# Performance work log

Hardware: AMD Instinct MI355X
Metric: run time of the kernel (lower is better)

The kernel has to match this reference:

```python
import jax, jax.numpy as jnp
import numpy as np

B, L, D, DA, NL = 32, 2048, 512, 512, 512

def setup_inputs() -> dict:
    key = jax.random.key(0)
    k1, k2, k3, k4 = jax.random.split(key, 4)
    std = 0.03
    return {
        "x": jax.random.normal(k1, (B, L, D), dtype=jnp.float32),
        "W1": jax.random.normal(k2, (DA, D), dtype=jnp.float32) * std,   # first_linears[0].weight [d_a, size]
        "W2": jax.random.normal(k3, (NL, DA), dtype=jnp.float32) * std,  # second_linears[0].weight [n_labels, d_a]
        "W3": jax.random.normal(k4, (NL, D), dtype=jnp.float32) * std,   # third_linears[0].weight [n_labels, size]
        "b3": jnp.zeros((NL,), dtype=jnp.float32),                        # third_linears[0].bias
    }

def reference(x, W1, W2, W3, b3):
    # weights = tanh(first_linear(x)) : [B, L, DA]
    w = jnp.tanh(jnp.einsum("bld,ad->bla", x, W1))
    # att logits : [B, L, NL]; softmax over seq dim (dim=1), then transpose -> [B, NL, L]
    att = jax.nn.softmax(jnp.einsum("bla,na->bln", w, W2), axis=1)
    att_weights = jnp.swapaxes(att, 1, 2)  # [B, NL, L]
    # context_vector = att_weights @ x : [B, NL, D]
    context_vector = jnp.einsum("bnl,bld->bnd", att_weights, x)
    # label-wise diagonal mul-sum-add: [B, NL]
    weighted_output = jnp.einsum("bnd,nd->bn", context_vector, W3) + b3
    return (context_vector, weighted_output, att_weights)
```

## Files before the change

kernel.cpp:

```cpp
#include <hip/hip_runtime.h>
#include <math.h>

#define BB 32
#define LL 2048
#define DD 512
#define DA_ 512
#define NL_ 512

typedef __bf16 bf16;
typedef __bf16 bf16x8 __attribute__((ext_vector_type(8)));
typedef __bf16 bf16x4 __attribute__((ext_vector_type(4)));
typedef float floatx4 __attribute__((ext_vector_type(4)));

__device__ __forceinline__ void dma16(const void* g, void* l) {
    __builtin_amdgcn_global_load_lds((__attribute__((address_space(1))) void*)g,
                                     (__attribute__((address_space(3))) void*)l,
                                     16, 0, 0);
}

__device__ __forceinline__ float fast_tanh(float x) {
    const float e = __expf(2.f * x);
    return 1.f - 2.f * __builtin_amdgcn_rcpf(e + 1.f);
}

__device__ __forceinline__ void gemm_core(const bf16* __restrict__ A,
                                          const bf16* __restrict__ B,
                                          int K, int lda, int ldb,
                                          floatx4 acc[4][4])
{
    __shared__ bf16 As[2][128 * 32];
    __shared__ bf16 Bs[2][128 * 32];
    const int tid = threadIdx.x;
    const int lane = tid & 63, wv = tid >> 6;
    const int wr = wv >> 1, wc = wv & 1;
    const int lm = lane & 15, quad = lane >> 4;

    const bf16* a0 = A + (size_t)(tid >> 2) * lda + (tid & 3) * 8;
    const bf16* b0 = B + (size_t)(tid >> 2) * ldb + (tid & 3) * 8;
    const size_t a1 = (size_t)64 * lda, b1 = (size_t)64 * ldb;

    dma16(a0,      &As[0][tid * 8]);
    dma16(a0 + a1, &As[0][2048 + tid * 8]);
    dma16(b0,      &Bs[0][tid * 8]);
    dma16(b0 + b1, &Bs[0][2048 + tid * 8]);
    __syncthreads();

    const int nk = K >> 5;
    for (int t = 0; t < nk; ++t) {
        const int cur = t & 1;
        if (t + 1 < nk) {
            const int k0 = (t + 1) << 5;
            dma16(a0 + k0,      &As[cur ^ 1][tid * 8]);
            dma16(a0 + a1 + k0, &As[cur ^ 1][2048 + tid * 8]);
            dma16(b0 + k0,      &Bs[cur ^ 1][tid * 8]);
            dma16(b0 + b1 + k0, &Bs[cur ^ 1][2048 + tid * 8]);
        }
        bf16x8 af[4], bfr[4];
        #pragma unroll
        for (int tt = 0; tt < 4; ++tt) {
            af[tt]  = *(const bf16x8*)(&As[cur][(wr * 64 + tt * 16 + lm) * 32 + quad * 8]);
            bfr[tt] = *(const bf16x8*)(&Bs[cur][(wc * 64 + tt * 16 + lm) * 32 + quad * 8]);
        }
        __builtin_amdgcn_s_setprio(1);
        #pragma unroll
        for (int i = 0; i < 4; ++i)
            #pragma unroll
            for (int j = 0; j < 4; ++j)
                acc[i][j] = __builtin_amdgcn_mfma_f32_16x16x32_bf16(af[i], bfr[j], acc[i][j], 0, 0, 0);
        __builtin_amdgcn_s_setprio(0);
        __syncthreads();
    }
}

__global__ __launch_bounds__(256) void k_cvt(const float* __restrict__ src,
                                             bf16* __restrict__ dst, int n)
{
    const int i = (blockIdx.x * 256 + threadIdx.x) * 4;
    if (i < n) {
        const float4 v = *(const float4*)(src + i);
        bf16x4 p = {(bf16)v.x, (bf16)v.y, (bf16)v.z, (bf16)v.w};
        *(bf16x4*)(dst + i) = p;
    }
}

__global__ __launch_bounds__(256) void k_init_wo(const float* __restrict__ b3,
                                                 float* __restrict__ wo)
{
    const int i = blockIdx.x * 256 + threadIdx.x;
    wo[i] = b3[i & (NL_ - 1)];
}

__global__ __launch_bounds__(256) void k_transpose(const float* __restrict__ x,
                                                   bf16* __restrict__ xT,
                                                   bf16* __restrict__ xb)
{
    __shared__ float T[64][68];
    const int b = blockIdx.z;
    const int l0 = blockIdx.x * 64, d0 = blockIdx.y * 64;
    const int tid = threadIdx.x;
    const float* xsrc = x + ((size_t)b * LL + l0) * DD + d0;
    bf16* xbdst = xb + ((size_t)b * LL + l0) * DD + d0;
    #pragma unroll
    for (int it = 0; it < 4; ++it) {
        const int c = tid + it * 256;
        const int lr = c >> 4, cc = (c & 15) * 4;
        const float4 v = *(const float4*)(xsrc + (size_t)lr * DD + cc);
        T[lr][cc] = v.x; T[lr][cc + 1] = v.y; T[lr][cc + 2] = v.z; T[lr][cc + 3] = v.w;
        bf16x4 p = {(bf16)v.x, (bf16)v.y, (bf16)v.z, (bf16)v.w};
        *(bf16x4*)(xbdst + (size_t)lr * DD + cc) = p;
    }
    __syncthreads();
    const int dl = tid >> 2, ls = (tid & 3) * 16;
    bf16x8 p0, p1;
    #pragma unroll
    for (int j = 0; j < 8; ++j) p0[j] = (bf16)T[ls + j][dl];
    #pragma unroll
    for (int j = 0; j < 8; ++j) p1[j] = (bf16)T[ls + 8 + j][dl];
    bf16* o = xT + ((size_t)b * DD + d0 + dl) * LL + l0 + ls;
    *(bf16x8*)o = p0;
    *(bf16x8*)(o + 8) = p1;
}

__global__ __launch_bounds__(256) void k_gemm1(const bf16* __restrict__ xb,
                                               const bf16* __restrict__ W1b,
                                               bf16* __restrict__ wb)
{
    const int n0 = blockIdx.x * 128;
    const size_t m0 = (size_t)blockIdx.y * 128;
    floatx4 acc[4][4];
    #pragma unroll
    for (int i = 0; i < 4; ++i)
        #pragma unroll
        for (int j = 0; j < 4; ++j) { floatx4 z = {0.f, 0.f, 0.f, 0.f}; acc[i][j] = z; }
    gemm_core(xb + m0 * DD, W1b + (size_t)n0 * DD, DD, DD, DD, acc);

    const int tid = threadIdx.x, lane = tid & 63, wv = tid >> 6;
    const int wr = wv >> 1, wc = wv & 1, lm = lane & 15, quad = lane >> 4;
    const size_t row0 = m0 + wr * 64 + quad * 4;
    const int col0 = n0 + wc * 64 + lm;
    #pragma unroll
    for (int i = 0; i < 4; ++i)
        #pragma unroll
        for (int j = 0; j < 4; ++j)
            #pragma unroll
            for (int r = 0; r < 4; ++r)
                wb[(row0 + i * 16 + r) * DA_ + col0 + j * 16] = (bf16)fast_tanh(acc[i][j][r]);
}

__global__ __launch_bounds__(256) void k_gemm2(const bf16* __restrict__ wb,
                                               const bf16* __restrict__ W2b,
                                               bf16* __restrict__ logitsb)
{
    const int c0 = blockIdx.x * 128;
    const int m0 = blockIdx.y * 128;
    floatx4 acc[4][4];
    #pragma unroll
    for (int i = 0; i < 4; ++i)
        #pragma unroll
        for (int j = 0; j < 4; ++j) { floatx4 z = {0.f, 0.f, 0.f, 0.f}; acc[i][j] = z; }
    gemm_core(W2b + (size_t)m0 * DA_, wb + (size_t)c0 * DA_, DA_, DA_, DA_, acc);

    const int b = c0 >> 11, lloc = c0 & (LL - 1);
    const int tid = threadIdx.x, lane = tid & 63, wv = tid >> 6;
    const int wr = wv >> 1, wc = wv & 1, lm = lane & 15, quad = lane >> 4;
    bf16* base = logitsb + ((size_t)b * NL_ + m0 + wr * 64 + quad * 4) * LL
               + lloc + wc * 64 + lm;
    #pragma unroll
    for (int i = 0; i < 4; ++i)
        #pragma unroll
        for (int j = 0; j < 4; ++j)
            #pragma unroll
            for (int r = 0; r < 4; ++r)
                base[(size_t)(i * 16 + r) * LL + j * 16] = (bf16)acc[i][j][r];
}

__global__ __launch_bounds__(256) void k_softmax(const bf16* __restrict__ logitsb,
                                                 float* __restrict__ att,
                                                 bf16* __restrict__ attb)
{
    const int tid = threadIdx.x;
    const bf16* p = logitsb + (size_t)blockIdx.x * LL;
    float* po = att + (size_t)blockIdx.x * LL;
    bf16* pb = attb + (size_t)blockIdx.x * LL;

    const bf16x8 v = *(const bf16x8*)(p + tid * 8);
    float f[8];
    #pragma unroll
    for (int j = 0; j < 8; ++j) f[j] = (float)v[j];

    __shared__ float red[8];
    float m = f[0];
    #pragma unroll
    for (int j = 1; j < 8; ++j) m = fmaxf(m, f[j]);
    #pragma unroll
    for (int off = 32; off; off >>= 1) m = fmaxf(m, __shfl_down(m, off));
    if ((tid & 63) == 0) red[tid >> 6] = m;
    __syncthreads();
    m = fmaxf(fmaxf(red[0], red[1]), fmaxf(red[2], red[3]));

    float s = 0.f;
    #pragma unroll
    for (int j = 0; j < 8; ++j) { f[j] = __expf(f[j] - m); s += f[j]; }
    #pragma unroll
    for (int off = 32; off; off >>= 1) s += __shfl_down(s, off);
    if ((tid & 63) == 0) red[4 + (tid >> 6)] = s;
    __syncthreads();
    s = red[4] + red[5] + red[6] + red[7];

    const float inv = 1.0f / s;
    float4 o0, o1;
    o0.x = f[0] * inv; o0.y = f[1] * inv; o0.z = f[2] * inv; o0.w = f[3] * inv;
    o1.x = f[4] * inv; o1.y = f[5] * inv; o1.z = f[6] * inv; o1.w = f[7] * inv;
    *(float4*)(po + tid * 8) = o0;
    *(float4*)(po + tid * 8 + 4) = o1;
    bf16x8 q = {(bf16)o0.x, (bf16)o0.y, (bf16)o0.z, (bf16)o0.w,
                (bf16)o1.x, (bf16)o1.y, (bf16)o1.z, (bf16)o1.w};
    *(bf16x8*)(pb + tid * 8) = q;
}

__global__ __launch_bounds__(256) void k_gemm3(const bf16* __restrict__ attb,
                                               const bf16* __restrict__ xT,
                                               float* __restrict__ ctx,
                                               const float* __restrict__ W3,
                                               float* __restrict__ wo)
{
    const int b = blockIdx.z;
    const int n0 = blockIdx.x * 128;
    const int m0 = blockIdx.y * 128;
    floatx4 acc[4][4];
    #pragma unroll
    for (int i = 0; i < 4; ++i)
        #pragma unroll
        for (int j = 0; j < 4; ++j) { floatx4 z = {0.f, 0.f, 0.f, 0.f}; acc[i][j] = z; }
    gemm_core(attb + ((size_t)b * NL_ + m0) * LL,
              xT + ((size_t)b * DD + n0) * LL, LL, LL, LL, acc);

    const int tid = threadIdx.x, lane = tid & 63, wv = tid >> 6;
    const int wr = wv >> 1, wc = wv & 1, lm = lane & 15, quad = lane >> 4;
    float* base = ctx + ((size_t)b * NL_ + m0 + wr * 64 + quad * 4) * DD
                + n0 + wc * 64 + lm;
    #pragma unroll
    for (int i = 0; i < 4; ++i)
        #pragma unroll
        for (int j = 0; j < 4; ++j)
            #pragma unroll
            for (int r = 0; r < 4; ++r)
                base[(size_t)(i * 16 + r) * DD + j * 16] = acc[i][j][r];

    const int nbase = m0 + wr * 64 + quad * 4;
    const int dbase = n0 + wc * 64 + lm;
    #pragma unroll
    for (int i = 0; i < 4; ++i) {
        #pragma unroll
        for (int r = 0; r < 4; ++r) {
            const int n = nbase + i * 16 + r;
            float s = 0.f;
            #pragma unroll
            for (int j = 0; j < 4; ++j)
                s += acc[i][j][r] * W3[(size_t)n * DD + dbase + j * 16];
            #pragma unroll
            for (int off = 8; off; off >>= 1) s += __shfl_down(s, off);
            if (lm == 0) atomicAdd(&wo[(size_t)b * NL_ + n], s);
        }
    }
}

extern "C" void kernel_launch(void* const* d_in, const int* in_sizes, int n_in,
                              void* d_out, int out_size, void* d_ws, size_t ws_size,
                              hipStream_t stream)
{
    const float* x  = (const float*)d_in[0];
    const float* W1 = (const float*)d_in[1];
    const float* W2 = (const float*)d_in[2];
    const float* W3 = (const float*)d_in[3];
    const float* b3 = (const float*)d_in[4];

    float* out = (float*)d_out;
    float* ctx = out;
    float* wo  = out + (size_t)BB * NL_ * DD;
    float* att = wo + (size_t)BB * NL_;

    char* wsp = (char*)d_ws;
    const size_t M64 = (size_t)64 * 1024 * 1024;
    bf16* xT      = (bf16*)(wsp);
    bf16* xb      = (bf16*)(wsp + M64);
    bf16* logitsb = (bf16*)(wsp + M64);
    bf16* wb      = (bf16*)(wsp + 2 * M64);
    bf16* attb    = (bf16*)(wsp + 2 * M64);
    bf16* W1b     = (bf16*)(wsp + 3 * M64);
    bf16* W2b     = W1b + (size_t)DA_ * DD;

    k_cvt<<<(DA_ * DD) / 1024, 256, 0, stream>>>(W1, W1b, DA_ * DD);
    k_cvt<<<(NL_ * DA_) / 1024, 256, 0, stream>>>(W2, W2b, NL_ * DA_);
    k_init_wo<<<(BB * NL_) / 256, 256, 0, stream>>>(b3, wo);
    k_transpose<<<dim3(LL / 64, DD / 64, BB), 256, 0, stream>>>(x, xT, xb);
    k_gemm1<<<dim3(DA_ / 128, (BB * LL) / 128), 256, 0, stream>>>(xb, W1b, wb);
    k_gemm2<<<dim3((BB * LL) / 128, NL_ / 128), 256, 0, stream>>>(wb, W2b, logitsb);
    k_softmax<<<BB * NL_, 256, 0, stream>>>(logitsb, att, attb);
    k_gemm3<<<dim3(DD / 128, NL_ / 128, BB), 256, 0, stream>>>(attb, xT, ctx, W3, wo);
}
```

Before: 522.7 us.

## Reorganize GEMM LDS tile layout k-major and swizzle blocks across XCDs

Changes the shared-memory tile layout so each 8-element k-chunk is stored row-contiguous by k-quarter. MFMA fragment reads then hit consecutive 16-byte slots across lanes instead of strided 64-byte rows, which is meant to reduce LDS bank conflicts. Separately, all three GEMMs now use a 1D grid remapped so that consecutive tiles sharing operands land on the same XCD, which is meant to improve L2 reuse. The 2D/3D grids are replaced by flat launch counts with manual index decoding, so any error in the decode would silently compute the wrong tiles.

```diff
diff --git a/kernel.cpp b/kernel.cpp
--- a/kernel.cpp
+++ b/kernel.cpp
@@ -35,14 +35,14 @@
     const int wr = wv >> 1, wc = wv & 1;
     const int lm = lane & 15, quad = lane >> 4;
 
-    const bf16* a0 = A + (size_t)(tid >> 2) * lda + (tid & 3) * 8;
-    const bf16* b0 = B + (size_t)(tid >> 2) * ldb + (tid & 3) * 8;
-    const size_t a1 = (size_t)64 * lda, b1 = (size_t)64 * ldb;
-
-    dma16(a0,      &As[0][tid * 8]);
-    dma16(a0 + a1, &As[0][2048 + tid * 8]);
-    dma16(b0,      &Bs[0][tid * 8]);
-    dma16(b0 + b1, &Bs[0][2048 + tid * 8]);
+    const int row = tid & 127, kq0 = tid >> 7;
+    const bf16* aP = A + (size_t)row * lda + kq0 * 8;
+    const bf16* bP = B + (size_t)row * ldb + kq0 * 8;
+
+    dma16(aP,      &As[0][tid * 8]);
+    dma16(aP + 16, &As[0][2048 + tid * 8]);
+    dma16(bP,      &Bs[0][tid * 8]);
+    dma16(bP + 16, &Bs[0][2048 + tid * 8]);
     __syncthreads();
 
     const int nk = K >> 5;
@@ -50,16 +50,16 @@
         const int cur = t & 1;
         if (t + 1 < nk) {
             const int k0 = (t + 1) << 5;
-            dma16(a0 + k0,      &As[cur ^ 1][tid * 8]);
-            dma16(a0 + a1 + k0, &As[cur ^ 1][2048 + tid * 8]);
-            dma16(b0 + k0,      &Bs[cur ^ 1][tid * 8]);
-            dma16(b0 + b1 + k0, &Bs[cur ^ 1][2048 + tid * 8]);
+            dma16(aP + k0,      &As[cur ^ 1][tid * 8]);
+            dma16(aP + k0 + 16, &As[cur ^ 1][2048 + tid * 8]);
+            dma16(bP + k0,      &Bs[cur ^ 1][tid * 8]);
+            dma16(bP + k0 + 16, &Bs[cur ^ 1][2048 + tid * 8]);
         }
         bf16x8 af[4], bfr[4];
         #pragma unroll
         for (int tt = 0; tt < 4; ++tt) {
-            af[tt]  = *(const bf16x8*)(&As[cur][(wr * 64 + tt * 16 + lm) * 32 + quad * 8]);
-            bfr[tt] = *(const bf16x8*)(&Bs[cur][(wc * 64 + tt * 16 + lm) * 32 + quad * 8]);
+            af[tt]  = *(const bf16x8*)(&As[cur][(quad * 128 + wr * 64 + tt * 16 + lm) * 8]);
+            bfr[tt] = *(const bf16x8*)(&Bs[cur][(quad * 128 + wc * 64 + tt * 16 + lm) * 8]);
         }
         __builtin_amdgcn_s_setprio(1);
         #pragma unroll
@@ -70,6 +70,10 @@
         __builtin_amdgcn_s_setprio(0);
         __syncthreads();
     }
+}
+
+__device__ __forceinline__ int xcd_swz(int bid, int chunk_log2) {
+    return ((bid & 7) << chunk_log2) | (bid >> 3);
 }
 
 __global__ __launch_bounds__(256) void k_cvt(const float* __restrict__ src,
@@ -125,8 +129,9 @@
                                                const bf16* __restrict__ W1b,
                                                bf16* __restrict__ wb)
 {
-    const int n0 = blockIdx.x * 128;
-    const size_t m0 = (size_t)blockIdx.y * 128;
+    const int w = xcd_swz(blockIdx.x, 8);
+    const int n0 = (w & 3) * 128;
+    const size_t m0 = (size_t)(w >> 2) * 128;
     floatx4 acc[4][4];
     #pragma unroll
     for (int i = 0; i < 4; ++i)
@@ -151,8 +156,9 @@
                                                const bf16* __restrict__ W2b,
                                                bf16* __restrict__ logitsb)
 {
-    const int c0 = blockIdx.x * 128;
-    const int m0 = blockIdx.y * 128;
+    const int w = xcd_swz(blockIdx.x, 8);
+    const int c0 = (w >> 2) * 128;
+    const int m0 = (w & 3) * 128;
     floatx4 acc[4][4];
     #pragma unroll
     for (int i = 0; i < 4; ++i)
@@ -224,9 +230,10 @@
                                                const float* __restrict__ W3,
                                                float* __restrict__ wo)
 {
-    const int b = blockIdx.z;
-    const int n0 = blockIdx.x * 128;
-    const int m0 = blockIdx.y * 128;
+    const int w = xcd_swz(blockIdx.x, 6);
+    const int b  = w >> 4;
+    const int m0 = ((w >> 2) & 3) * 128;
+    const int n0 = (w & 3) * 128;
     floatx4 acc[4][4];
     #pragma unroll
     for (int i = 0; i < 4; ++i)
@@ -294,8 +301,8 @@
     k_cvt<<<(NL_ * DA_) / 1024, 256, 0, stream>>>(W2, W2b, NL_ * DA_);
     k_init_wo<<<(BB * NL_) / 256, 256, 0, stream>>>(b3, wo);
     k_transpose<<<dim3(LL / 64, DD / 64, BB), 256, 0, stream>>>(x, xT, xb);
-    k_gemm1<<<dim3(DA_ / 128, (BB * LL) / 128), 256, 0, stream>>>(xb, W1b, wb);
-    k_gemm2<<<dim3((BB * LL) / 128, NL_ / 128), 256, 0, stream>>>(wb, W2b, logitsb);
+    k_gemm1<<<2048, 256, 0, stream>>>(xb, W1b, wb);
+    k_gemm2<<<2048, 256, 0, stream>>>(wb, W2b, logitsb);
     k_softmax<<<BB * NL_, 256, 0, stream>>>(logitsb, att, attb);
-    k_gemm3<<<dim3(DD / 128, NL_ / 128, BB), 256, 0, stream>>>(attb, xT, ctx, W3, wo);
-}
+    k_gemm3<<<512, 256, 0, stream>>>(attb, xT, ctx, W3, wo);
+}
```

Result: slower. 578.1 us (+10.6%).
